# Kernel optimization log

Hardware: AMD Instinct MI355X
Metric: run time of the kernel (lower is better)

Reference implementation:

```python
import jax, jax.numpy as jnp
import numpy as np

B, D, N, C = 4096, 2048, 8, 1024  # batch, in_features, ncomponents, per-component out channels


def setup_inputs() -> dict:
    key = jax.random.key(0)
    k1, k2, k3, k4 = jax.random.split(key, 4)
    scale_w = 1.0 / np.sqrt(D)
    return {
        "x": jax.random.normal(k1, (B, D), dtype=jnp.float32),
        "W": jax.random.normal(k2, (N, C, D), dtype=jnp.float32) * scale_w,
        "b": jax.random.normal(k3, (N, C), dtype=jnp.float32) * scale_w,
        "Wg_w": jax.random.normal(k4, (D, 1), dtype=jnp.float32) * scale_w,
        "Wg_b": jnp.zeros((1,), dtype=jnp.float32),
    }


def reference(x, W, b, Wg_w, Wg_b):
    n = W.shape[0]
    # scalar gate per sample: g in [0, ncomponents]
    g = n * 0.5 * (1.0 + jnp.tanh(x @ Wg_w + Wg_b))            # [B, 1]
    k = jnp.floor(g)                                            # [B, 1]
    idx = jnp.arange(n, dtype=x.dtype)[None, :]                 # [1, N]
    M_hard = (idx <= k).astype(x.dtype)                        # monotonic prefix mask [B, N]
    # straight-through estimator: forward = hard mask, grad wrt g = sum over components
    M = jax.lax.stop_gradient(M_hard - g) + g                   # [B, N]
    # L1 normalize (torch fn.normalize p=1, eps=1e-12)
    G = M / jnp.maximum(jnp.sum(jnp.abs(M), axis=1, keepdims=True), 1e-12)
    # all component outputs; unselected components have G==0 so they contribute the
    # same zeros the original pads with (equal-width components, out = N*C)
    Y = jnp.einsum('bd,ncd->bnc', x, W) + b                     # [B, N, C]
    E = (G[:, :, None] * Y).reshape(x.shape[0], -1)             # [B, N*C]
    return E, G
```

## Files before the change

kernel.cpp:

```cpp
#include <hip/hip_runtime.h>
#include <hip/hip_bf16.h>

#define BATCH 4096
#define DK    2048
#define NCOMP 8
#define NC    8192
#define NT    (DK / 64)

typedef unsigned int u32;
typedef unsigned short u16;
typedef short bf16x8 __attribute__((ext_vector_type(8)));
typedef float f32x4 __attribute__((ext_vector_type(4)));

__device__ __forceinline__ u16 f2bf(float f) {
    union { float f; u32 u; } v; v.f = f;
    u32 r = v.u + 0x7fffu + ((v.u >> 16) & 1u);
    return (u16)(r >> 16);
}

__global__ void cvtW_kernel(const float* __restrict__ in, u16* __restrict__ out) {
    int i = blockIdx.x * blockDim.x + threadIdx.x;
    float4 a = ((const float4*)in)[i];
    ushort4 o = { f2bf(a.x), f2bf(a.y), f2bf(a.z), f2bf(a.w) };
    ((ushort4*)out)[i] = o;
}

__global__ __launch_bounds__(256)
void xgate_kernel(const float* __restrict__ x, const float* __restrict__ wg,
                  const float* __restrict__ wgb, u16* __restrict__ xb,
                  float* __restrict__ G) {
    int row = blockIdx.x;
    int t = threadIdx.x;
    const float4* xr = (const float4*)(x + (size_t)row * DK);
    const float4* wr = (const float4*)wg;
    float4 a = xr[t], b = xr[t + 256];
    float4 wa = wr[t], wb = wr[t + 256];
    float s = a.x*wa.x + a.y*wa.y + a.z*wa.z + a.w*wa.w
            + b.x*wb.x + b.y*wb.y + b.z*wb.z + b.w*wb.w;
    ushort4 o1 = { f2bf(a.x), f2bf(a.y), f2bf(a.z), f2bf(a.w) };
    ushort4 o2 = { f2bf(b.x), f2bf(b.y), f2bf(b.z), f2bf(b.w) };
    ushort4* xo = (ushort4*)(xb + (size_t)row * DK);
    xo[t] = o1;
    xo[t + 256] = o2;
    __shared__ float red[4];
#pragma unroll
    for (int off = 32; off; off >>= 1) s += __shfl_xor(s, off, 64);
    if ((t & 63) == 0) red[t >> 6] = s;
    __syncthreads();
    if (t == 0) {
        float sum = (red[0] + red[1]) + (red[2] + red[3]);
        float g = 0.5f * (float)NCOMP * (1.0f + tanhf(sum + wgb[0]));
        float k = floorf(g);
        float mh[NCOMP]; float den = 0.f;
#pragma unroll
        for (int n = 0; n < NCOMP; ++n) {
            float m = ((float)n <= k) ? 1.0f : 0.0f;
            m = (m - g) + g;
            mh[n] = m; den += fabsf(m);
        }
        den = fmaxf(den, 1e-12f);
#pragma unroll
        for (int n = 0; n < NCOMP; ++n) G[(size_t)row * NCOMP + n] = mh[n] / den;
    }
}

__device__ __forceinline__ void stage_half(const u16* __restrict__ gbase,
                                           u16* __restrict__ ldsHalf, int tid) {
#pragma unroll
    for (int i = 0; i < 2; ++i) {
        int c = tid + i * 512;
        int row = c >> 3;
        int slot = (c & 7) ^ (row & 7);
        const u16* src = gbase + (size_t)row * DK + slot * 8;
        u16* dst = ldsHalf + (size_t)(c >> 6) * 512;
        __builtin_amdgcn_global_load_lds((const __attribute__((address_space(1))) u32*)src,
                                         (__attribute__((address_space(3))) u32*)dst, 16, 0, 0);
    }
}

__device__ __forceinline__ bf16x8 frag(const u16* __restrict__ h, int lrow, int slot) {
    return *(const bf16x8*)(h + lrow * 64 + ((slot ^ (lrow & 7)) << 3));
}

#define PH_MID()  do { __builtin_amdgcn_s_barrier(); \
    asm volatile("s_waitcnt lgkmcnt(0)" ::: "memory"); \
    __builtin_amdgcn_sched_barrier(0); \
    __builtin_amdgcn_s_setprio(1); } while (0)
#define PH_END()  do { __builtin_amdgcn_s_setprio(0); \
    __builtin_amdgcn_s_barrier(); } while (0)

__global__ __launch_bounds__(512, 2)
void gemm_kernel(const u16* __restrict__ A, const u16* __restrict__ Bw,
                 const float* __restrict__ bias, const float* __restrict__ Gtab,
                 float* __restrict__ E) {
    __shared__ u16 lds[2][2][2][128 * 64];
    int tid = threadIdx.x;
    int l = tid & 63;
    int w = tid >> 6;
    int wr = w >> 2, wc = w & 3;
    int r16 = l & 15, kg = l >> 4;

    int bid = blockIdx.x;
    int swz = (bid & 7) * 64 + (bid >> 3);
    int brow = (swz >> 5) * 256;
    int bcol = (swz & 31) * 256;

    f32x4 acc[8][4] = {};

    const u16* gA = A + (size_t)brow * DK;
    const u16* gB = Bw + (size_t)bcol * DK;

    stage_half(gA,                 lds[0][0][0], tid);
    stage_half(gA + 128 * DK,      lds[0][0][1], tid);
    stage_half(gB,                 lds[0][1][0], tid);
    stage_half(gB + 128 * DK,      lds[0][1][1], tid);
    stage_half(gB + 64,            lds[1][1][0], tid);
    stage_half(gB + 128 * DK + 64, lds[1][1][1], tid);
    stage_half(gA + 64,            lds[1][0][0], tid);
    asm volatile("s_waitcnt vmcnt(6)" ::: "memory");
    __builtin_amdgcn_s_barrier();

    for (int t = 0; t < NT; ++t) {
        int p = t & 1;
        const u16* Ah = lds[p][0][wr];
        const u16* Bh = lds[p][1][wc >> 1];
        int brB = (wc & 1) * 64;
        bool pf1 = (t + 1) < NT;
        bool pf2 = (t + 2) < NT;
        int koff1 = (t + 1) * 64;
        int koff2 = (t + 2) * 64;

        bf16x8 aF[4][2], aG[4][2], bF[2][2], bG[2][2];

#pragma unroll
        for (int j = 0; j < 4; ++j)
#pragma unroll
            for (int kk = 0; kk < 2; ++kk)
                aF[j][kk] = frag(Ah, j * 16 + r16, kk * 4 + kg);
#pragma unroll
        for (int jn = 0; jn < 2; ++jn)
#pragma unroll
            for (int kk = 0; kk < 2; ++kk)
                bF[jn][kk] = frag(Bh, brB + jn * 16 + r16, kk * 4 + kg);
        if (pf1) stage_half(gA + 128 * DK + koff1, lds[p ^ 1][0][1], tid);
        PH_MID();
#pragma unroll
        for (int j = 0; j < 4; ++j)
#pragma unroll
            for (int jn = 0; jn < 2; ++jn)
#pragma unroll
                for (int kk = 0; kk < 2; ++kk)
                    acc[j][jn] = __builtin_amdgcn_mfma_f32_16x16x32_bf16(aF[j][kk], bF[jn][kk], acc[j][jn], 0, 0, 0);
        PH_END();

#pragma unroll
        for (int jn = 0; jn < 2; ++jn)
#pragma unroll
            for (int kk = 0; kk < 2; ++kk)
                bG[jn][kk] = frag(Bh, brB + 32 + jn * 16 + r16, kk * 4 + kg);
        PH_MID();
#pragma unroll
        for (int j = 0; j < 4; ++j)
#pragma unroll
            for (int jn = 0; jn < 2; ++jn)
#pragma unroll
                for (int kk = 0; kk < 2; ++kk)
                    acc[j][2 + jn] = __builtin_amdgcn_mfma_f32_16x16x32_bf16(aF[j][kk], bG[jn][kk], acc[j][2 + jn], 0, 0, 0);
        PH_END();

#pragma unroll
        for (int j = 0; j < 4; ++j)
#pragma unroll
            for (int kk = 0; kk < 2; ++kk)
                aG[j][kk] = frag(Ah, 64 + j * 16 + r16, kk * 4 + kg);
        if (pf2) stage_half(gB + koff2, lds[p][1][0], tid);
        PH_MID();
#pragma unroll
        for (int j = 0; j < 4; ++j)
#pragma unroll
            for (int jn = 0; jn < 2; ++jn)
#pragma unroll
                for (int kk = 0; kk < 2; ++kk)
                    acc[4 + j][2 + jn] = __builtin_amdgcn_mfma_f32_16x16x32_bf16(aG[j][kk], bG[jn][kk], acc[4 + j][2 + jn], 0, 0, 0);
        PH_END();

        if (pf2) {
            stage_half(gB + 128 * DK + koff2, lds[p][1][1], tid);
            stage_half(gA + koff2,            lds[p][0][0], tid);
        }
        PH_MID();
#pragma unroll
        for (int j = 0; j < 4; ++j)
#pragma unroll
            for (int jn = 0; jn < 2; ++jn)
#pragma unroll
                for (int kk = 0; kk < 2; ++kk)
                    acc[4 + j][jn] = __builtin_amdgcn_mfma_f32_16x16x32_bf16(aG[j][kk], bF[jn][kk], acc[4 + j][jn], 0, 0, 0);
        __builtin_amdgcn_s_setprio(0);
        if (pf2)      asm volatile("s_waitcnt vmcnt(6)" ::: "memory");
        else if (pf1) asm volatile("s_waitcnt vmcnt(0)" ::: "memory");
        if (pf1) __builtin_amdgcn_s_barrier();
    }

    int ncomp = (bcol + wc * 64) >> 10;
    int rbase = brow + wr * 128;
    int cbase = bcol + wc * 64;
    float bs[4];
#pragma unroll
    for (int ni = 0; ni < 4; ++ni) bs[ni] = bias[cbase + ni * 16 + r16];
#pragma unroll
    for (int mi = 0; mi < 8; ++mi)
#pragma unroll
        for (int r = 0; r < 4; ++r) {
            int row = rbase + mi * 16 + kg * 4 + r;
            float gv = Gtab[(size_t)row * NCOMP + ncomp];
            float* Erow = E + (size_t)row * NC + cbase;
#pragma unroll
            for (int ni = 0; ni < 4; ++ni)
                Erow[ni * 16 + r16] = gv * (acc[mi][ni][r] + bs[ni]);
        }
}

extern "C" void kernel_launch(void* const* d_in, const int* in_sizes, int n_in,
                              void* d_out, int out_size, void* d_ws, size_t ws_size,
                              hipStream_t stream) {
    const float* x   = (const float*)d_in[0];
    const float* W   = (const float*)d_in[1];
    const float* b   = (const float*)d_in[2];
    const float* wgw = (const float*)d_in[3];
    const float* wgb = (const float*)d_in[4];
    float* E = (float*)d_out;
    float* G = E + (size_t)BATCH * NC;

    u16* xb = (u16*)d_ws;
    u16* Wb = xb + (size_t)BATCH * DK;

    cvtW_kernel<<<NC * DK / 4 / 256, 256, 0, stream>>>(W, Wb);
    xgate_kernel<<<BATCH, 256, 0, stream>>>(x, wgw, wgb, xb, G);
    gemm_kernel<<<(BATCH / 256) * (NC / 256), 512, 0, stream>>>(xb, Wb, b, G, E);
}
```

Baseline: 326.8 us.

## Software-pipeline LDS fragment loads across phases with precomputed swizzled addresses

Restructures the GEMM main loop into a templated tile body with prologue and epilogue specializations. The next tile's A fragments are loaded during the last MFMA phase of the current tile, B fragments are loaded together, and partial lgkmcnt waits replace full waits. Swizzled LDS and global offsets are computed once outside the loop, and the per-iteration prefetch branches are removed. The aim is to hide LDS read latency behind MFMA and cut address arithmetic, at the cost of more live registers and a hand-tuned wait-count scheme that is fragile to get right.

```diff
diff --git a/kernel.cpp b/kernel.cpp
--- a/kernel.cpp
+++ b/kernel.cpp
@@ -11,6 +11,8 @@
 typedef unsigned short u16;
 typedef short bf16x8 __attribute__((ext_vector_type(8)));
 typedef float f32x4 __attribute__((ext_vector_type(4)));
+#define AS1 __attribute__((address_space(1)))
+#define AS3 __attribute__((address_space(3)))
 
 __device__ __forceinline__ u16 f2bf(float f) {
     union { float f; u32 u; } v; v.f = f;
@@ -64,40 +66,105 @@
     }
 }
 
-__device__ __forceinline__ void stage_half(const u16* __restrict__ gbase,
-                                           u16* __restrict__ ldsHalf, int tid) {
-#pragma unroll
-    for (int i = 0; i < 2; ++i) {
-        int c = tid + i * 512;
-        int row = c >> 3;
-        int slot = (c & 7) ^ (row & 7);
-        const u16* src = gbase + (size_t)row * DK + slot * 8;
-        u16* dst = ldsHalf + (size_t)(c >> 6) * 512;
-        __builtin_amdgcn_global_load_lds((const __attribute__((address_space(1))) u32*)src,
-                                         (__attribute__((address_space(3))) u32*)dst, 16, 0, 0);
-    }
-}
-
-__device__ __forceinline__ bf16x8 frag(const u16* __restrict__ h, int lrow, int slot) {
-    return *(const bf16x8*)(h + lrow * 64 + ((slot ^ (lrow & 7)) << 3));
-}
-
-#define PH_MID()  do { __builtin_amdgcn_s_barrier(); \
-    asm volatile("s_waitcnt lgkmcnt(0)" ::: "memory"); \
-    __builtin_amdgcn_sched_barrier(0); \
-    __builtin_amdgcn_s_setprio(1); } while (0)
-#define PH_END()  do { __builtin_amdgcn_s_setprio(0); \
-    __builtin_amdgcn_s_barrier(); } while (0)
+
+#define BAR()        __builtin_amdgcn_s_barrier()
+#define SCHED0()     __builtin_amdgcn_sched_barrier(0)
+#define PRIO(N)      __builtin_amdgcn_s_setprio(N)
+#define WAIT_LGKM(N) asm volatile("s_waitcnt lgkmcnt(" #N ")" ::: "memory")
+#define WAIT_VM(N)   asm volatile("s_waitcnt vmcnt(" #N ")" ::: "memory")
+
+#define STAGE(usrc, dhalf) do { \
+    __builtin_amdgcn_global_load_lds((const AS1 u32*)((usrc) + go0), (AS3 u32*)((dhalf) + d0), 16, 0, 0); \
+    __builtin_amdgcn_global_load_lds((const AS1 u32*)((usrc) + go1), (AS3 u32*)((dhalf) + d1), 16, 0, 0); \
+  } while (0)
+
+#define MFQ(MB, NB, AFR, BFR) \
+  do { _Pragma("unroll") for (int j = 0; j < 4; ++j) \
+       _Pragma("unroll") for (int jn = 0; jn < 2; ++jn) \
+       _Pragma("unroll") for (int kk = 0; kk < 2; ++kk) \
+         acc[(MB) + j][(NB) + jn] = __builtin_amdgcn_mfma_f32_16x16x32_bf16( \
+             AFR[j][kk], BFR[jn][kk], acc[(MB) + j][(NB) + jn], 0, 0, 0); } while (0)
+
+template<int MODE>
+__device__ __forceinline__ void tile_body(
+    const u16* Ab0, const u16* Ab1, const u16* Bb0, const u16* Bb1,
+    const u16* nAb0, const u16* nAb1,
+    const u16* uA1n, const u16* uB0, const u16* uB1, const u16* uA0,
+    u16* dA1n, u16* dB0, u16* dB1, u16* dA0,
+    u32 go0, u32 go1, int d0, int d1,
+    bf16x8 (&aF)[4][2], bf16x8 (&aG)[4][2], bf16x8 (&bF)[2][2], bf16x8 (&bG)[2][2],
+    f32x4 (&acc)[8][4])
+{
+    if (MODE <= 1) STAGE(uA1n, dA1n);
+#pragma unroll
+    for (int jn = 0; jn < 2; ++jn) {
+        bF[jn][0] = *(const bf16x8*)(Bb0 + jn * 1024);
+        bF[jn][1] = *(const bf16x8*)(Bb1 + jn * 1024);
+    }
+    SCHED0();
+#pragma unroll
+    for (int jn = 0; jn < 2; ++jn) {
+        bG[jn][0] = *(const bf16x8*)(Bb0 + 2048 + jn * 1024);
+        bG[jn][1] = *(const bf16x8*)(Bb1 + 2048 + jn * 1024);
+    }
+    BAR();
+    WAIT_LGKM(4);
+    SCHED0(); PRIO(1);
+    MFQ(0, 0, aF, bF);
+    PRIO(0); BAR();
+
+#pragma unroll
+    for (int j = 0; j < 4; ++j) {
+        aG[j][0] = *(const bf16x8*)(Ab0 + 4096 + j * 1024);
+        aG[j][1] = *(const bf16x8*)(Ab1 + 4096 + j * 1024);
+    }
+    BAR();
+    WAIT_LGKM(8);
+    SCHED0(); PRIO(1);
+    MFQ(0, 2, aF, bG);
+    PRIO(0); BAR();
+
+    if (MODE == 0) STAGE(uB0, dB0);
+    BAR();
+    WAIT_LGKM(0);
+    SCHED0(); PRIO(1);
+    MFQ(4, 2, aG, bG);
+    PRIO(0); BAR();
+
+    if (MODE == 0) {
+        WAIT_VM(2);
+        STAGE(uB1, dB1);
+        STAGE(uA0, dA0);
+    } else if (MODE == 1) {
+        WAIT_VM(0);
+    }
+    BAR();
+    if (MODE != 2) {
+#pragma unroll
+        for (int j = 0; j < 4; ++j) {
+            aF[j][0] = *(const bf16x8*)(nAb0 + j * 1024);
+            aF[j][1] = *(const bf16x8*)(nAb1 + j * 1024);
+        }
+        WAIT_LGKM(8);
+    } else {
+        WAIT_LGKM(0);
+    }
+    SCHED0(); PRIO(1);
+    MFQ(4, 0, aG, bF);
+    PRIO(0);
+    if (MODE != 2) BAR();
+}
 
 __global__ __launch_bounds__(512, 2)
 void gemm_kernel(const u16* __restrict__ A, const u16* __restrict__ Bw,
                  const float* __restrict__ bias, const float* __restrict__ Gtab,
                  float* __restrict__ E) {
-    __shared__ u16 lds[2][2][2][128 * 64];
+    __shared__ u16 lds[2 * 32768];
     int tid = threadIdx.x;
     int l = tid & 63;
     int w = tid >> 6;
     int wr = w >> 2, wc = w & 3;
+    int wcB = wc >> 1, brB = (wc & 1) * 64;
     int r16 = l & 15, kg = l >> 4;
 
     int bid = blockIdx.x;
@@ -106,100 +173,68 @@
     int bcol = (swz & 31) * 256;
 
     f32x4 acc[8][4] = {};
+    bf16x8 aF[4][2], aG[4][2], bF[2][2], bG[2][2];
 
     const u16* gA = A + (size_t)brow * DK;
     const u16* gB = Bw + (size_t)bcol * DK;
 
-    stage_half(gA,                 lds[0][0][0], tid);
-    stage_half(gA + 128 * DK,      lds[0][0][1], tid);
-    stage_half(gB,                 lds[0][1][0], tid);
-    stage_half(gB + 128 * DK,      lds[0][1][1], tid);
-    stage_half(gB + 64,            lds[1][1][0], tid);
-    stage_half(gB + 128 * DK + 64, lds[1][1][1], tid);
-    stage_half(gA + 64,            lds[1][0][0], tid);
-    asm volatile("s_waitcnt vmcnt(6)" ::: "memory");
-    __builtin_amdgcn_s_barrier();
-
-    for (int t = 0; t < NT; ++t) {
-        int p = t & 1;
-        const u16* Ah = lds[p][0][wr];
-        const u16* Bh = lds[p][1][wc >> 1];
-        int brB = (wc & 1) * 64;
-        bool pf1 = (t + 1) < NT;
-        bool pf2 = (t + 2) < NT;
-        int koff1 = (t + 1) * 64;
-        int koff2 = (t + 2) * 64;
-
-        bf16x8 aF[4][2], aG[4][2], bF[2][2], bG[2][2];
-
-#pragma unroll
-        for (int j = 0; j < 4; ++j)
-#pragma unroll
-            for (int kk = 0; kk < 2; ++kk)
-                aF[j][kk] = frag(Ah, j * 16 + r16, kk * 4 + kg);
-#pragma unroll
-        for (int jn = 0; jn < 2; ++jn)
-#pragma unroll
-            for (int kk = 0; kk < 2; ++kk)
-                bF[jn][kk] = frag(Bh, brB + jn * 16 + r16, kk * 4 + kg);
-        if (pf1) stage_half(gA + 128 * DK + koff1, lds[p ^ 1][0][1], tid);
-        PH_MID();
-#pragma unroll
-        for (int j = 0; j < 4; ++j)
-#pragma unroll
-            for (int jn = 0; jn < 2; ++jn)
-#pragma unroll
-                for (int kk = 0; kk < 2; ++kk)
-                    acc[j][jn] = __builtin_amdgcn_mfma_f32_16x16x32_bf16(aF[j][kk], bF[jn][kk], acc[j][jn], 0, 0, 0);
-        PH_END();
-
-#pragma unroll
-        for (int jn = 0; jn < 2; ++jn)
-#pragma unroll
-            for (int kk = 0; kk < 2; ++kk)
-                bG[jn][kk] = frag(Bh, brB + 32 + jn * 16 + r16, kk * 4 + kg);
-        PH_MID();
-#pragma unroll
-        for (int j = 0; j < 4; ++j)
-#pragma unroll
-            for (int jn = 0; jn < 2; ++jn)
-#pragma unroll
-                for (int kk = 0; kk < 2; ++kk)
-                    acc[j][2 + jn] = __builtin_amdgcn_mfma_f32_16x16x32_bf16(aF[j][kk], bG[jn][kk], acc[j][2 + jn], 0, 0, 0);
-        PH_END();
-
-#pragma unroll
-        for (int j = 0; j < 4; ++j)
-#pragma unroll
-            for (int kk = 0; kk < 2; ++kk)
-                aG[j][kk] = frag(Ah, 64 + j * 16 + r16, kk * 4 + kg);
-        if (pf2) stage_half(gB + koff2, lds[p][1][0], tid);
-        PH_MID();
-#pragma unroll
-        for (int j = 0; j < 4; ++j)
-#pragma unroll
-            for (int jn = 0; jn < 2; ++jn)
-#pragma unroll
-                for (int kk = 0; kk < 2; ++kk)
-                    acc[4 + j][2 + jn] = __builtin_amdgcn_mfma_f32_16x16x32_bf16(aG[j][kk], bG[jn][kk], acc[4 + j][2 + jn], 0, 0, 0);
-        PH_END();
-
-        if (pf2) {
-            stage_half(gB + 128 * DK + koff2, lds[p][1][1], tid);
-            stage_half(gA + koff2,            lds[p][0][0], tid);
-        }
-        PH_MID();
-#pragma unroll
-        for (int j = 0; j < 4; ++j)
-#pragma unroll
-            for (int jn = 0; jn < 2; ++jn)
-#pragma unroll
-                for (int kk = 0; kk < 2; ++kk)
-                    acc[4 + j][jn] = __builtin_amdgcn_mfma_f32_16x16x32_bf16(aG[j][kk], bF[jn][kk], acc[4 + j][jn], 0, 0, 0);
-        __builtin_amdgcn_s_setprio(0);
-        if (pf2)      asm volatile("s_waitcnt vmcnt(6)" ::: "memory");
-        else if (pf1) asm volatile("s_waitcnt vmcnt(0)" ::: "memory");
-        if (pf1) __builtin_amdgcn_s_barrier();
+    int c1 = tid + 512;
+    u32 go0 = (u32)((tid >> 3) * DK + (((tid & 7) ^ ((tid >> 3) & 7)) * 8));
+    u32 go1 = (u32)((c1 >> 3) * DK + (((c1 & 7) ^ ((c1 >> 3) & 7)) * 8));
+    int d0 = w * 512, d1 = w * 512 + 4096;
+
+    int swb = r16 * 64;
+    int sw0 = ((kg) ^ (r16 & 7)) * 8;
+    int sw1 = ((4 + kg) ^ (r16 & 7)) * 8;
+    const u16* Ab0_ = lds + wr * 8192 + swb + sw0;
+    const u16* Ab1_ = lds + wr * 8192 + swb + sw1;
+    const u16* Bb0_ = lds + 16384 + wcB * 8192 + brB * 64 + swb + sw0;
+    const u16* Bb1_ = lds + 16384 + wcB * 8192 + brB * 64 + swb + sw1;
+
+    STAGE(gA,                 lds);
+    STAGE(gA + 128 * DK,      lds + 8192);
+    STAGE(gB,                 lds + 16384);
+    STAGE(gB + 128 * DK,      lds + 24576);
+    STAGE(gB + 64,            lds + 32768 + 16384);
+    STAGE(gB + 128 * DK + 64, lds + 32768 + 24576);
+    STAGE(gA + 64,            lds + 32768);
+    WAIT_VM(6);
+    BAR();
+#pragma unroll
+    for (int j = 0; j < 4; ++j) {
+        aF[j][0] = *(const bf16x8*)(Ab0_ + j * 1024);
+        aF[j][1] = *(const bf16x8*)(Ab1_ + j * 1024);
+    }
+
+#pragma unroll 1
+    for (int t = 0; t <= NT - 3; ++t) {
+        u32 cbo = (u32)(t & 1) * 32768, nbo = cbo ^ 32768;
+        tile_body<0>(Ab0_ + cbo, Ab1_ + cbo, Bb0_ + cbo, Bb1_ + cbo,
+                     Ab0_ + nbo, Ab1_ + nbo,
+                     gA + 128 * DK + (size_t)(t + 1) * 64,
+                     gB + (size_t)(t + 2) * 64,
+                     gB + 128 * DK + (size_t)(t + 2) * 64,
+                     gA + (size_t)(t + 2) * 64,
+                     lds + nbo + 8192, lds + cbo + 16384, lds + cbo + 24576, lds + cbo,
+                     go0, go1, d0, d1, aF, aG, bF, bG, acc);
+    }
+    {
+        int t = NT - 2;
+        u32 cbo = (u32)(t & 1) * 32768, nbo = cbo ^ 32768;
+        tile_body<1>(Ab0_ + cbo, Ab1_ + cbo, Bb0_ + cbo, Bb1_ + cbo,
+                     Ab0_ + nbo, Ab1_ + nbo,
+                     gA + 128 * DK + (size_t)(t + 1) * 64, gB, gB, gA,
+                     lds + nbo + 8192, lds + cbo + 16384, lds + cbo + 24576, lds + cbo,
+                     go0, go1, d0, d1, aF, aG, bF, bG, acc);
+    }
+    {
+        int t = NT - 1;
+        u32 cbo = (u32)(t & 1) * 32768, nbo = cbo ^ 32768;
+        tile_body<2>(Ab0_ + cbo, Ab1_ + cbo, Bb0_ + cbo, Bb1_ + cbo,
+                     Ab0_ + nbo, Ab1_ + nbo,
+                     gA, gB, gB, gA,
+                     lds + nbo + 8192, lds + cbo + 16384, lds + cbo + 24576, lds + cbo,
+                     go0, go1, d0, d1, aF, aG, bF, bG, acc);
     }
 
     int ncomp = (bcol + wc * 64) >> 10;
```

Result: no change. 327.7 us (+0.3%).
